# Kernel optimization log

Hardware: AMD Instinct MI355X
Metric: run time of the kernel (lower is better)

## Reference

```python
import jax, jax.numpy as jnp
import numpy as np

B, H, I, E = 4096, 1024, 4096, 8
TOP_K = 2


def setup_inputs() -> dict:
    key = jax.random.key(0)
    ks = jax.random.split(key, 8)
    s = 0.02
    return {
        "x": jax.random.normal(ks[0], (B, H), jnp.float32),
        "noise": -jnp.log(-jnp.log(jax.random.uniform(ks[1], (B, E), jnp.float32) + 1e-20) + 1e-20),
        "Wr": jax.random.normal(ks[2], (H, E), jnp.float32) * s,
        "br": jnp.zeros((E,), jnp.float32),
        "W_in": jax.random.normal(ks[3], (E, H, 2 * I), jnp.float32) * s,
        "b_in": jnp.zeros((E, 2 * I), jnp.float32),
        "W_out": jax.random.normal(ks[4], (E, I, H), jnp.float32) * s,
        "b_out": jnp.zeros((E, H), jnp.float32),
    }


def reference(x, noise, Wr, br, W_in, b_in, W_out, b_out):
    # Router + Gumbel top-2 (temperature = 1.0)
    logits = x @ Wr + br                      # [B, E]
    y = logits + noise
    vals, idxs = jax.lax.top_k(y, TOP_K)      # [B, 2]
    w = jax.nn.softmax(vals, axis=-1)         # softmax over the 2 selected vals
    # Dense gate matrix: gates[b, e] = sum_k w[b,k] * (idxs[b,k] == e)
    onehot = (idxs[:, :, None] == jnp.arange(E)[None, None, :]).astype(x.dtype)  # [B,2,E]
    gates = jnp.einsum("bk,bke->be", w, onehot)                                   # [B,E]

    out = jnp.zeros_like(x)
    for e in range(E):  # small static expert loop
        h = x @ W_in[e] + b_in[e]             # [B, 2I]
        x1, x2 = jnp.split(h, 2, axis=-1)     # SwiGLU: chunk(2, dim=-1)
        a = x1 * jax.nn.sigmoid(x2)           # [B, I]
        o = a @ W_out[e] + b_out[e]           # [B, H]
        out = out + gates[:, e:e + 1] * o
    # dropout is identity in eval mode
    return out
```

## Files before the change

### kernel.cpp

```cpp
#include <hip/hip_runtime.h>

#define B_TOK 4096
#define HDIM 1024
#define IDIM 4096
#define NSLOT 8192
#define MAX_T128 72
#define G1_BLOCKS (8 * MAX_T128 * 8)

using short8   = __attribute__((ext_vector_type(8))) short;
using bf16x8   = __attribute__((ext_vector_type(8))) __bf16;
using f32x4    = __attribute__((ext_vector_type(4))) float;
using int4v    = __attribute__((ext_vector_type(4))) int;
using ushort4v = __attribute__((ext_vector_type(4))) unsigned short;
using float4v  = __attribute__((ext_vector_type(4))) float;

#define MC_NT128   0
#define MC_E128    8
#define MC_M0128   80
#define MC_RW128   152
#define META_INTS  256

__device__ __forceinline__ unsigned short f2bf(float f) {
  unsigned u = __float_as_uint(f);
  u += 0x7FFFu + ((u >> 16) & 1u);
  return (unsigned short)(u >> 16);
}
__device__ __forceinline__ float bf2f(unsigned short h) {
  return __uint_as_float(((unsigned)h) << 16);
}
__device__ __forceinline__ f32x4 mfma_bf16(short8 a, short8 b, f32x4 c) {
  return __builtin_amdgcn_mfma_f32_16x16x32_bf16(
      __builtin_bit_cast(bf16x8, a), __builtin_bit_cast(bf16x8, b), c, 0, 0, 0);
}
__device__ __forceinline__ void gload16(const unsigned short* g, unsigned short* l) {
  __builtin_amdgcn_global_load_lds(
      (const __attribute__((address_space(1))) unsigned int*)g,
      (__attribute__((address_space(3))) unsigned int*)l, 16, 0, 0);
}

__device__ __forceinline__ void prep_wout_body(
    const float* __restrict__ W_out, unsigned short* __restrict__ Wt,
    int bx, int by, int e, unsigned short* T, int tid) {
  int k0 = by * 64, n0 = bx * 64;
#pragma unroll
  for (int i = 0; i < 4; i++) {
    int q = i * 256 + tid;
    int kr = q >> 4, nc = (q & 15) * 4;
    float4v v = *(const float4v*)(W_out + ((size_t)e * 4096 + k0 + kr) * 1024 + n0 + nc);
#pragma unroll
    for (int j = 0; j < 4; j++) T[(nc + j) * 72 + kr] = f2bf(v[j]);
  }
  __syncthreads();
  unsigned short* ob = Wt + ((size_t)e * 1024 + n0) * 4096;
#pragma unroll
  for (int i = 0; i < 2; i++) {
    int q = i * 256 + tid;
    int nr = q >> 3, kc = (q & 7) * 8;
    *(int4v*)(ob + (size_t)nr * 4096 + k0 + kc) = *(const int4v*)&T[nr * 72 + kc];
  }
}

__global__ __launch_bounds__(256) void fused_pre_kernel(
    const float* __restrict__ x, const float* __restrict__ noise,
    const float* __restrict__ Wr, const float* __restrict__ br,
    int* __restrict__ idxmap, float* __restrict__ wmap,
    const float* __restrict__ W_in, unsigned short* __restrict__ Wt,
    unsigned short* __restrict__ x_bf) {
  __shared__ __align__(16) unsigned short T[64 * 72];
  int bid = blockIdx.x;
  int tid = threadIdx.x;
  if (bid < 1024) {
    int tok = bid * 4 + (tid >> 6);
    int l = tid & 63;
    const float* xr = x + (size_t)tok * HDIM;
    float acc[8];
#pragma unroll
    for (int e = 0; e < 8; e++) acc[e] = 0.f;
    for (int hb = 0; hb < HDIM; hb += 256) {
      int h = hb + l * 4;
      float4v xv = *(const float4v*)(xr + h);
#pragma unroll
      for (int j = 0; j < 4; j++) {
        float4v w0 = *(const float4v*)(Wr + (size_t)(h + j) * 8);
        float4v w1 = *(const float4v*)(Wr + (size_t)(h + j) * 8 + 4);
        acc[0] += xv[j] * w0[0]; acc[1] += xv[j] * w0[1];
        acc[2] += xv[j] * w0[2]; acc[3] += xv[j] * w0[3];
        acc[4] += xv[j] * w1[0]; acc[5] += xv[j] * w1[1];
        acc[6] += xv[j] * w1[2]; acc[7] += xv[j] * w1[3];
      }
    }
#pragma unroll
    for (int off = 32; off > 0; off >>= 1) {
#pragma unroll
      for (int e = 0; e < 8; e++) acc[e] += __shfl_xor(acc[e], off, 64);
    }
    if (l == 0) {
      float y[8];
#pragma unroll
      for (int e = 0; e < 8; e++) y[e] = acc[e] + br[e] + noise[(size_t)tok * 8 + e];
      int e0 = 0;
#pragma unroll
      for (int e = 1; e < 8; e++) if (y[e] > y[e0]) e0 = e;
      int e1 = (e0 == 0) ? 1 : 0;
#pragma unroll
      for (int e = 0; e < 8; e++) if (e != e0 && y[e] > y[e1]) e1 = e;
      float w0 = 1.f / (1.f + __expf(y[e1] - y[e0]));
      idxmap[tok * 2] = e0; idxmap[tok * 2 + 1] = e1;
      wmap[tok * 2] = w0;   wmap[tok * 2 + 1] = 1.f - w0;
    }
    return;
  }
  if (bid >= 17408) {
    int flat = (bid - 17408) * 2048 + tid * 8;
    float4v v0 = *(const float4v*)(x + flat);
    float4v v1 = *(const float4v*)(x + flat + 4);
    int4v p;
    p[0] = (int)((unsigned)f2bf(v0[0]) | ((unsigned)f2bf(v0[1]) << 16));
    p[1] = (int)((unsigned)f2bf(v0[2]) | ((unsigned)f2bf(v0[3]) << 16));
    p[2] = (int)((unsigned)f2bf(v1[0]) | ((unsigned)f2bf(v1[1]) << 16));
    p[3] = (int)((unsigned)f2bf(v1[2]) | ((unsigned)f2bf(v1[3]) << 16));
    *(int4v*)(x_bf + flat) = p;
    return;
  }
  int pid = bid - 1024;
  int e = pid >> 11, rem = pid & 2047;
  int k0 = (rem >> 7) * 64, n0 = (rem & 127) * 64;
#pragma unroll
  for (int i = 0; i < 4; i++) {
    int q = i * 256 + tid;
    int kr = q >> 4, nc = (q & 15) * 4;
    float4v v = *(const float4v*)(W_in + ((size_t)e * 1024 + k0 + kr) * 8192 + n0 + nc);
#pragma unroll
    for (int j = 0; j < 4; j++) T[(nc + j) * 72 + kr] = f2bf(v[j]);
  }
  __syncthreads();
  int half = (n0 >= 4096) ? 1 : 0;
  int j0 = n0 - half * 4096;
  int J = j0 >> 6;
  unsigned short* ob = Wt + (((size_t)e * 64 + J) << 17);
#pragma unroll
  for (int i = 0; i < 2; i++) {
    int q = i * 256 + tid;
    int nr = q >> 3, kc = (q & 7) * 8;
    int pr = (nr >> 4) * 32 + half * 16 + (nr & 15);
    *(int4v*)(ob + (size_t)pr * 1024 + k0 + kc) = *(const int4v*)&T[nr * 72 + kc];
  }
}

__global__ __launch_bounds__(1024) void rank_kernel(
    const int* __restrict__ idxmap, int* __restrict__ slotmap,
    int* __restrict__ meta, int* __restrict__ inv) {
  int tid = threadIdx.x, lane = tid & 63, wv = tid >> 6;
  __shared__ unsigned wtot[16][4];
  __shared__ unsigned woff[16][4];
  __shared__ unsigned offE[8];

  int es[8];
  unsigned p0 = 0, p1 = 0, p2 = 0, p3 = 0;
#pragma unroll
  for (int j = 0; j < 8; j++) {
    int e = idxmap[tid * 8 + j];
    es[j] = e;
    unsigned c = 1u << ((e & 1) * 16);
    if (e < 2) p0 += c; else if (e < 4) p1 += c;
    else if (e < 6) p2 += c; else p3 += c;
  }
  unsigned i0 = p0, i1 = p1, i2 = p2, i3 = p3;
#pragma unroll
  for (int d = 1; d < 64; d <<= 1) {
    unsigned t0 = __shfl_up(i0, d, 64), t1 = __shfl_up(i1, d, 64);
    unsigned t2 = __shfl_up(i2, d, 64), t3 = __shfl_up(i3, d, 64);
    if (lane >= d) { i0 += t0; i1 += t1; i2 += t2; i3 += t3; }
  }
  if (lane == 63) { wtot[wv][0] = i0; wtot[wv][1] = i1; wtot[wv][2] = i2; wtot[wv][3] = i3; }
  __syncthreads();
  if (wv == 0 && lane < 16) {
    unsigned a0 = wtot[lane][0], a1 = wtot[lane][1], a2 = wtot[lane][2], a3 = wtot[lane][3];
    unsigned s0 = a0, s1 = a1, s2 = a2, s3 = a3;
#pragma unroll
    for (int d = 1; d < 16; d <<= 1) {
      unsigned t0 = __shfl_up(s0, d, 64), t1 = __shfl_up(s1, d, 64);
      unsigned t2 = __shfl_up(s2, d, 64), t3 = __shfl_up(s3, d, 64);
      if (lane >= d) { s0 += t0; s1 += t1; s2 += t2; s3 += t3; }
    }
    woff[lane][0] = s0 - a0; woff[lane][1] = s1 - a1;
    woff[lane][2] = s2 - a2; woff[lane][3] = s3 - a3;
    if (lane == 15) {
      unsigned t[8];
      t[0] = s0 & 0xFFFF; t[1] = s0 >> 16; t[2] = s1 & 0xFFFF; t[3] = s1 >> 16;
      t[4] = s2 & 0xFFFF; t[5] = s2 >> 16; t[6] = s3 & 0xFFFF; t[7] = s3 >> 16;
      unsigned off = 0; int tc = 0;
      for (int e = 0; e < 8; e++) {
        offE[e] = off;
        for (unsigned i = 0; i < t[e]; i += 128) {
          meta[MC_E128 + tc] = e;
          meta[MC_M0128 + tc] = (int)(off + i);
          meta[MC_RW128 + tc] = (int)((t[e] - i < 128u) ? (t[e] - i) : 128u);
          tc++;
        }
        off += t[e];
      }
      meta[MC_NT128] = tc;
    }
  }
  __syncthreads();
  unsigned e0w = i0 - p0 + woff[wv][0];
  unsigned e1w = i1 - p1 + woff[wv][1];
  unsigned e2w = i2 - p2 + woff[wv][2];
  unsigned e3w = i3 - p3 + woff[wv][3];
#pragma unroll
  for (int j = 0; j < 8; j++) {
    int e = es[j];
    unsigned sh = (unsigned)(e & 1) * 16;
    unsigned c = 1u << sh, v;
    if (e < 2)      { v = (e0w >> sh) & 0xFFFF; e0w += c; }
    else if (e < 4) { v = (e1w >> sh) & 0xFFFF; e1w += c; }
    else if (e < 6) { v = (e2w >> sh) & 0xFFFF; e2w += c; }
    else            { v = (e3w >> sh) & 0xFFFF; e3w += c; }
    int slot = (int)(offE[e] + v);
    slotmap[tid * 8 + j] = slot;
    inv[slot] = (tid * 8 + j) >> 1;
  }
}

__global__ __launch_bounds__(256) void prep_wout_kernel(
    const float* __restrict__ W_out, unsigned short* __restrict__ Wt) {
  __shared__ __align__(16) unsigned short T[64 * 72];
  prep_wout_body(W_out, Wt, blockIdx.x, blockIdx.y, blockIdx.z, T, threadIdx.x);
}

__global__ __launch_bounds__(256, 4) void gemm1a_kernel(
    const unsigned short* __restrict__ x_bf, const unsigned short* __restrict__ Wt,
    const float* __restrict__ b_in, unsigned short* __restrict__ a_buf,
    const int* __restrict__ meta, const int* __restrict__ inv,
    const float* __restrict__ W_out, unsigned short* __restrict__ Wot) {
  __shared__ __align__(16) unsigned short As[128 * 64];
  __shared__ __align__(16) unsigned short Bs[128 * 64];
  int bid = blockIdx.x;
  if (bid >= G1_BLOCKS) {
    int pid = bid - G1_BLOCKS;
    int e = pid >> 10, rem = pid & 1023;
    prep_wout_body(W_out, Wot, rem & 15, rem >> 4, e, As, threadIdx.x);
    return;
  }
  int xcd = bid & 7, local = bid >> 3;
  int t = local >> 3;
  if (t >= meta[MC_NT128]) return;
  int J = xcd * 8 + (local & 7);
  int e = meta[MC_E128 + t];
  int m0 = meta[MC_M0128 + t];
  int rows = meta[MC_RW128 + t];
  const unsigned short* Wp = Wt + (((size_t)e * 64 + J) << 17);

  int tid = threadIdx.x, l = tid & 63, w = tid >> 6;
  int g = l >> 4, ln = l & 15, lr = l >> 3;
  int uc = (l & 7) ^ lr;
  int wm = w >> 1, wn = w & 1;

  const unsigned short* sA[4]; const unsigned short* sB[4]; int dO[4];
#pragma unroll
  for (int i = 0; i < 4; i++) {
    int c = w * 4 + i;
    int r = c * 8 + lr;
    int ra = r < rows ? r : rows - 1;
    int tok = inv[m0 + ra];
    sA[i] = x_bf + (size_t)tok * HDIM + uc * 8;
    sB[i] = Wp + (size_t)r * 1024 + uc * 8;
    dO[i] = c * 512 + l * 8;
  }

  f32x4 acc[4][4];
#pragma unroll
  for (int mf = 0; mf < 4; mf++)
#pragma unroll
    for (int nf = 0; nf < 4; nf++) acc[mf][nf] = (f32x4){0.f, 0.f, 0.f, 0.f};

#pragma unroll 1
  for (int kt = 0; kt < 16; kt++) {
#pragma unroll
    for (int i = 0; i < 4; i++) gload16(sA[i] + kt * 64, &As[dO[i]]);
#pragma unroll
    for (int i = 0; i < 4; i++) gload16(sB[i] + kt * 64, &Bs[dO[i]]);
    __syncthreads();
#pragma unroll
    for (int ks = 0; ks < 2; ks++) {
      int u0 = (((ks * 4 + g) ^ (ln & 7)) << 3);
      short8 af[4], bfr[4];
#pragma unroll
      for (int mf = 0; mf < 4; mf++)
        af[mf] = *(const short8*)&As[(wm * 64 + mf * 16 + ln) * 64 + u0];
#pragma unroll
      for (int nf = 0; nf < 4; nf++)
        bfr[nf] = *(const short8*)&Bs[(wn * 64 + nf * 16 + ln) * 64 + u0];
#pragma unroll
      for (int mf = 0; mf < 4; mf++)
#pragma unroll
        for (int nf = 0; nf < 4; nf++)
          acc[mf][nf] = mfma_bf16(af[mf], bfr[nf], acc[mf][nf]);
    }
    __syncthreads();
  }
#pragma unroll
  for (int mf = 0; mf < 4; mf++) {
#pragma unroll
    for (int np = 0; np < 2; np++) {
      int j = J * 64 + wn * 32 + np * 16 + ln;
      float b1 = b_in[(size_t)e * 8192 + j];
      float b2 = b_in[(size_t)e * 8192 + 4096 + j];
#pragma unroll
      for (int r = 0; r < 4; r++) {
        int m = wm * 64 + mf * 16 + g * 4 + r;
        if (m < rows) {
          float h1 = acc[mf][np * 2][r] + b1;
          float h2 = acc[mf][np * 2 + 1][r] + b2;
          a_buf[(size_t)(m0 + m) * IDIM + j] = f2bf(h1 / (1.f + __expf(-h2)));
        }
      }
    }
  }
}

__global__ __launch_bounds__(256, 4) void gemm2a_kernel(
    const unsigned short* __restrict__ a_buf, const unsigned short* __restrict__ Wt,
    const float* __restrict__ b_out, unsigned short* __restrict__ buf2,
    const int* __restrict__ meta) {
  int bid = blockIdx.x;
  int xcd = bid & 7;
  int t = bid >> 3;
  if (t >= meta[MC_NT128]) return;
  int n0 = xcd * 128;
  int e = meta[MC_E128 + t];
  int m0 = meta[MC_M0128 + t];
  int rows = meta[MC_RW128 + t];
  const unsigned short* Wp = Wt + ((size_t)e * 1024 + n0) * 4096;

  __shared__ __align__(16) unsigned short As[128 * 64];
  __shared__ __align__(16) unsigned short Bs[128 * 64];

  int tid = threadIdx.x, l = tid & 63, w = tid >> 6;
  int g = l >> 4, ln = l & 15, lr = l >> 3;
  int uc = (l & 7) ^ lr;
  int wm = w >> 1, wn = w & 1;

  const unsigned short* sA[4]; const unsigned short* sB[4]; int dO[4];
#pragma unroll
  for (int i = 0; i < 4; i++) {
    int c = w * 4 + i;
    int r = c * 8 + lr;
    int ra = r < rows ? r : rows - 1;
    sA[i] = a_buf + (size_t)(m0 + ra) * IDIM + uc * 8;
    sB[i] = Wp + (size_t)r * 4096 + uc * 8;
    dO[i] = c * 512 + l * 8;
  }

  f32x4 acc[4][4];
#pragma unroll
  for (int mf = 0; mf < 4; mf++)
#pragma unroll
    for (int nf = 0; nf < 4; nf++) acc[mf][nf] = (f32x4){0.f, 0.f, 0.f, 0.f};

#pragma unroll 1
  for (int kt = 0; kt < 64; kt++) {
#pragma unroll
    for (int i = 0; i < 4; i++) gload16(sA[i] + kt * 64, &As[dO[i]]);
#pragma unroll
    for (int i = 0; i < 4; i++) gload16(sB[i] + kt * 64, &Bs[dO[i]]);
    __syncthreads();
#pragma unroll
    for (int ks = 0; ks < 2; ks++) {
      int u0 = (((ks * 4 + g) ^ (ln & 7)) << 3);
      short8 af[4], bfr[4];
#pragma unroll
      for (int mf = 0; mf < 4; mf++)
        af[mf] = *(const short8*)&As[(wm * 64 + mf * 16 + ln) * 64 + u0];
#pragma unroll
      for (int nf = 0; nf < 4; nf++)
        bfr[nf] = *(const short8*)&Bs[(wn * 64 + nf * 16 + ln) * 64 + u0];
#pragma unroll
      for (int mf = 0; mf < 4; mf++)
#pragma unroll
        for (int nf = 0; nf < 4; nf++)
          acc[mf][nf] = mfma_bf16(af[mf], bfr[nf], acc[mf][nf]);
    }
    __syncthreads();
  }
#pragma unroll
  for (int mf = 0; mf < 4; mf++) {
#pragma unroll
    for (int nf = 0; nf < 4; nf++) {
      int col = n0 + wn * 64 + nf * 16 + ln;
      float bo = b_out[(size_t)e * 1024 + col];
#pragma unroll
      for (int r = 0; r < 4; r++) {
        int m = wm * 64 + mf * 16 + g * 4 + r;
        if (m < rows) {
          buf2[(size_t)(m0 + m) * HDIM + col] = f2bf(acc[mf][nf][r] + bo);
        }
      }
    }
  }
}

__global__ __launch_bounds__(256) void combine_kernel(
    const unsigned short* __restrict__ buf2, const int* __restrict__ slotmap,
    const float* __restrict__ wmap, float* __restrict__ out) {
  int i = blockIdx.x * 256 + threadIdx.x;
  int base = i * 4;
  int b = base >> 10, h = base & 1023;
  int s0 = slotmap[b * 2], s1 = slotmap[b * 2 + 1];
  float w0 = wmap[b * 2], w1 = wmap[b * 2 + 1];
  ushort4v c0 = *(const ushort4v*)(buf2 + (size_t)s0 * HDIM + h);
  ushort4v c1 = *(const ushort4v*)(buf2 + (size_t)s1 * HDIM + h);
  float4v o;
#pragma unroll
  for (int j = 0; j < 4; j++) o[j] = w0 * bf2f(c0[j]) + w1 * bf2f(c1[j]);
  *(float4v*)(out + base) = o;
}

extern "C" void kernel_launch(void* const* d_in, const int* in_sizes, int n_in,
                              void* d_out, int out_size, void* d_ws, size_t ws_size,
                              hipStream_t stream) {
  const float* x     = (const float*)d_in[0];
  const float* noise = (const float*)d_in[1];
  const float* Wr    = (const float*)d_in[2];
  const float* br    = (const float*)d_in[3];
  const float* W_in  = (const float*)d_in[4];
  const float* b_in  = (const float*)d_in[5];
  const float* W_out = (const float*)d_in[6];
  const float* b_out = (const float*)d_in[7];
  float* out = (float*)d_out;
  char* ws = (char*)d_ws;

  const size_t NEED_B = 285343744ULL;
  bool big = (ws_size >= NEED_B);

  unsigned short* W_in_t  = (unsigned short*)ws;
  unsigned short* x_bf    = (unsigned short*)(ws + 134217728);
  unsigned short* buf2    = x_bf;
  unsigned short* a_buf   = (unsigned short*)(ws + 150994944);
  unsigned short* W_out_t = big ? (unsigned short*)(ws + 218103808)
                                : W_in_t;
  int* meta    = (int*)(ws + (big ? 285212672 : 218103808));
  int* idxmap  = meta + META_INTS;
  int* slotmap = idxmap + NSLOT;
  float* wmap  = (float*)(slotmap + NSLOT);
  int* inv     = idxmap;

  hipLaunchKernelGGL(fused_pre_kernel, dim3(1024 + 16384 + 2048), dim3(256), 0, stream,
                     x, noise, Wr, br, idxmap, wmap, W_in, W_in_t, x_bf);
  hipLaunchKernelGGL(rank_kernel, dim3(1), dim3(1024), 0, stream,
                     idxmap, slotmap, meta, inv);
  hipLaunchKernelGGL(gemm1a_kernel,
                     dim3(big ? (G1_BLOCKS + 8192) : G1_BLOCKS), dim3(256), 0, stream,
                     x_bf, W_in_t, b_in, a_buf, meta, inv, W_out, W_out_t);
  if (!big) {
    hipLaunchKernelGGL(prep_wout_kernel, dim3(16, 64, 8), dim3(256), 0, stream,
                       W_out, W_out_t);
  }
  hipLaunchKernelGGL(gemm2a_kernel, dim3(8 * MAX_T128), dim3(256), 0, stream,
                     a_buf, W_out_t, b_out, buf2, meta);
  hipLaunchKernelGGL(combine_kernel, dim3((B_TOK * HDIM / 4) / 256), dim3(256), 0, stream,
                     buf2, slotmap, wmap, out);
}
```

Before: 401.7 us.

## Swizzle transpose LDS tiles, interleave W_out prep with GEMM1 blocks, reorder pre-kernel

The transpose tiles used when converting W_in and W_out to bf16 now use an XOR swizzle in shared memory, to reduce LDS bank conflicts on the column-wise writes. In the big-workspace path, the W_out prep blocks are interleaved with GEMM1 tiles (9 GEMM groups per 16 prep groups) instead of being appended after them, so the bandwidth-bound conversion overlaps the compute-bound GEMM. The fused pre-kernel also moves the router blocks after the W_in transpose blocks in dispatch order. The cost is more complex block index mapping, and GEMM1 blocks may now compete with prep blocks for cache and bandwidth.

```diff
diff --git a/kernel.cpp b/kernel.cpp
--- a/kernel.cpp
+++ b/kernel.cpp
@@ -6,6 +6,7 @@
 #define NSLOT 8192
 #define MAX_T128 72
 #define G1_BLOCKS (8 * MAX_T128 * 8)
+#define G1_BIG_GRID 12800
 
 using short8   = __attribute__((ext_vector_type(8))) short;
 using bf16x8   = __attribute__((ext_vector_type(8))) __bf16;
@@ -48,15 +49,19 @@
     int kr = q >> 4, nc = (q & 15) * 4;
     float4v v = *(const float4v*)(W_out + ((size_t)e * 4096 + k0 + kr) * 1024 + n0 + nc);
 #pragma unroll
-    for (int j = 0; j < 4; j++) T[(nc + j) * 72 + kr] = f2bf(v[j]);
+    for (int j = 0; j < 4; j++) {
+      int rr = nc + j;
+      T[rr * 72 + ((((kr >> 3) ^ ((rr >> 2) & 7)) << 3) | (kr & 7))] = f2bf(v[j]);
+    }
   }
   __syncthreads();
   unsigned short* ob = Wt + ((size_t)e * 1024 + n0) * 4096;
 #pragma unroll
   for (int i = 0; i < 2; i++) {
     int q = i * 256 + tid;
-    int nr = q >> 3, kc = (q & 7) * 8;
-    *(int4v*)(ob + (size_t)nr * 4096 + k0 + kc) = *(const int4v*)&T[nr * 72 + kc];
+    int nr = q >> 3, u = q & 7;
+    int su = u ^ ((nr >> 2) & 7);
+    *(int4v*)(ob + (size_t)nr * 4096 + k0 + u * 8) = *(const int4v*)&T[nr * 72 + su * 8];
   }
 }
 
@@ -69,8 +74,8 @@
   __shared__ __align__(16) unsigned short T[64 * 72];
   int bid = blockIdx.x;
   int tid = threadIdx.x;
-  if (bid < 1024) {
-    int tok = bid * 4 + (tid >> 6);
+  if (bid >= 16384 && bid < 17408) {
+    int tok = (bid - 16384) * 4 + (tid >> 6);
     int l = tid & 63;
     const float* xr = x + (size_t)tok * HDIM;
     float acc[8];
@@ -122,7 +127,7 @@
     *(int4v*)(x_bf + flat) = p;
     return;
   }
-  int pid = bid - 1024;
+  int pid = bid;
   int e = pid >> 11, rem = pid & 2047;
   int k0 = (rem >> 7) * 64, n0 = (rem & 127) * 64;
 #pragma unroll
@@ -131,7 +136,10 @@
     int kr = q >> 4, nc = (q & 15) * 4;
     float4v v = *(const float4v*)(W_in + ((size_t)e * 1024 + k0 + kr) * 8192 + n0 + nc);
 #pragma unroll
-    for (int j = 0; j < 4; j++) T[(nc + j) * 72 + kr] = f2bf(v[j]);
+    for (int j = 0; j < 4; j++) {
+      int rr = nc + j;
+      T[rr * 72 + ((((kr >> 3) ^ ((rr >> 2) & 7)) << 3) | (kr & 7))] = f2bf(v[j]);
+    }
   }
   __syncthreads();
   int half = (n0 >= 4096) ? 1 : 0;
@@ -141,9 +149,10 @@
 #pragma unroll
   for (int i = 0; i < 2; i++) {
     int q = i * 256 + tid;
-    int nr = q >> 3, kc = (q & 7) * 8;
+    int nr = q >> 3, u = q & 7;
+    int su = u ^ ((nr >> 2) & 7);
     int pr = (nr >> 4) * 32 + half * 16 + (nr & 15);
-    *(int4v*)(ob + (size_t)pr * 1024 + k0 + kc) = *(const int4v*)&T[nr * 72 + kc];
+    *(int4v*)(ob + (size_t)pr * 1024 + k0 + u * 8) = *(const int4v*)&T[nr * 72 + su * 8];
   }
 }
 
@@ -237,16 +246,24 @@
   __shared__ __align__(16) unsigned short As[128 * 64];
   __shared__ __align__(16) unsigned short Bs[128 * 64];
   int bid = blockIdx.x;
-  if (bid >= G1_BLOCKS) {
-    int pid = bid - G1_BLOCKS;
-    int e = pid >> 10, rem = pid & 1023;
-    prep_wout_body(W_out, Wot, rem & 15, rem >> 4, e, As, threadIdx.x);
-    return;
-  }
-  int xcd = bid & 7, local = bid >> 3;
-  int t = local >> 3;
+  int xcd = bid & 7;
+  int gs;
+  if (gridDim.x == G1_BIG_GRID) {
+    int s = bid >> 3;
+    int gp = s / 25, r = s - gp * 25;
+    if (r >= 9) {
+      int pid = (gp * 16 + (r - 9)) * 8 + xcd;
+      int e = pid >> 10, rem = pid & 1023;
+      prep_wout_body(W_out, Wot, rem & 15, rem >> 4, e, As, threadIdx.x);
+      return;
+    }
+    gs = gp * 9 + r;
+  } else {
+    gs = bid >> 3;
+  }
+  int t = gs >> 3;
   if (t >= meta[MC_NT128]) return;
-  int J = xcd * 8 + (local & 7);
+  int J = xcd * 8 + (gs & 7);
   int e = meta[MC_E128 + t];
   int m0 = meta[MC_M0128 + t];
   int rows = meta[MC_RW128 + t];
@@ -446,12 +463,12 @@
   float* wmap  = (float*)(slotmap + NSLOT);
   int* inv     = idxmap;
 
-  hipLaunchKernelGGL(fused_pre_kernel, dim3(1024 + 16384 + 2048), dim3(256), 0, stream,
+  hipLaunchKernelGGL(fused_pre_kernel, dim3(16384 + 1024 + 2048), dim3(256), 0, stream,
                      x, noise, Wr, br, idxmap, wmap, W_in, W_in_t, x_bf);
   hipLaunchKernelGGL(rank_kernel, dim3(1), dim3(1024), 0, stream,
                      idxmap, slotmap, meta, inv);
   hipLaunchKernelGGL(gemm1a_kernel,
-                     dim3(big ? (G1_BLOCKS + 8192) : G1_BLOCKS), dim3(256), 0, stream,
+                     dim3(big ? G1_BIG_GRID : G1_BLOCKS), dim3(256), 0, stream,
                      x_bf, W_in_t, b_in, a_buf, meta, inv, W_out, W_out_t);
   if (!big) {
     hipLaunchKernelGGL(prep_wout_kernel, dim3(16, 64, 8), dim3(256), 0, stream,
```

Measured after the change: 403.5 us. Within noise of the previous version (+0.5%).
